# Kernel optimization log

Hardware: AMD Instinct MI355X
Metric: run time of the kernel (lower is better)

The kernel has to match this reference:

```python
import jax, jax.numpy as jnp
import numpy as np

B, N, DIM = 256, 196, 384
H, KD, VD = 12, 32, 32
RES = 14
EPS = 1e-5


def _build_bias_idxs():
    pts = [(i, j) for i in range(RES) for j in range(RES)]
    offs, idxs = {}, []
    for p1 in pts:
        for p2 in pts:
            o = (abs(p1[0] - p2[0]), abs(p1[1] - p2[1]))
            if o not in offs:
                offs[o] = len(offs)
            idxs.append(offs[o])
    return jnp.asarray(np.array(idxs, dtype=np.int32).reshape(N, N))


def setup_inputs() -> dict:
    key = jax.random.key(0)
    ks = jax.random.split(key, 4)
    return {
        "x": jax.random.normal(ks[0], (B, N, DIM), dtype=jnp.float32),
        "norm_w": jnp.ones((DIM,), jnp.float32),
        "norm_b": jnp.zeros((DIM,), jnp.float32),
        "qkv_w": jax.random.normal(ks[1], (H * (VD + 2 * KD), DIM), jnp.float32) * 0.02,
        "qkv_b": jnp.zeros((H * (VD + 2 * KD),), jnp.float32),
        "attention_biases": jax.random.normal(ks[2], (H, RES * RES), jnp.float32) * 0.02,
        "proj_w": jax.random.normal(ks[3], (DIM, H * VD), jnp.float32) * 0.02,
        "proj_b": jnp.zeros((DIM,), jnp.float32),
        "bias_idxs": _build_bias_idxs(),
    }


def reference(x, norm_w, norm_b, qkv_w, qkv_b, attention_biases, proj_w, proj_b, bias_idxs):
    scale = KD ** -0.5
    # LayerNorm over feature dim
    mu = jnp.mean(x, axis=-1, keepdims=True)
    var = jnp.mean(jnp.square(x - mu), axis=-1, keepdims=True)
    xn = (x - mu) * jax.lax.rsqrt(var + EPS) * norm_w + norm_b
    # QKV projection: [B,N,H*(2*KD+VD)] -> [B,N,H,*]
    qkv = (jnp.einsum("bnd,fd->bnf", xn, qkv_w) + qkv_b).reshape(B, N, H, 2 * KD + VD)
    q, k, v = qkv[..., :KD], qkv[..., KD:2 * KD], qkv[..., 2 * KD:]
    # Relative-position bias gathered into [H,N,N]
    attn_bias = attention_biases[:, bias_idxs]
    # Scores [B,H,N,N] with bias, softmax, AV
    scores = jnp.einsum("bnhk,bmhk->bhnm", q * scale, k) + attn_bias
    probs = jax.nn.softmax(scores, axis=-1)
    out = jnp.einsum("bhnm,bmhv->bnhv", probs, v).reshape(B, N, H * VD)
    return jnp.einsum("bnf,df->bnd", out, proj_w) + proj_b
```

## Files before the change

kernel.cpp:

```cpp
#include <hip/hip_runtime.h>

#define B_    256
#define N_    196
#define NP_   208
#define VSTR_ 264
#define DIM_  384
#define H_    12
#define KD_   32
#define VD_   32
#define F_    1152
#define ROWS_ (B_ * N_)
#define SCALE_ 0.17677669529663687f
#define EPS_  1e-5f

typedef __bf16 bf16_t;
typedef __bf16 bf16x2 __attribute__((ext_vector_type(2)));
typedef __bf16 bf16x4 __attribute__((ext_vector_type(4)));
typedef __bf16 bf16x8 __attribute__((ext_vector_type(8)));
typedef float  f32x4  __attribute__((ext_vector_type(4)));

__device__ __forceinline__ f32x4 mfma16(bf16x8 a, bf16x8 b, f32x4 c) {
    return __builtin_amdgcn_mfma_f32_16x16x32_bf16(a, b, c, 0, 0, 0);
}

__device__ __forceinline__ void gl2lds(const bf16_t* g, bf16_t* l) {
    __builtin_amdgcn_global_load_lds(
        (const __attribute__((address_space(1))) void*)g,
        (__attribute__((address_space(3))) void*)l, 16, 0, 0);
}

__global__ __launch_bounds__(256) void cvt_w(const float* __restrict__ src,
                                             bf16_t* __restrict__ dst) {
    const int i = (blockIdx.x * 256 + threadIdx.x) * 4;
    const float4 v = *(const float4*)(src + i);
    bf16x4 o = {(bf16_t)v.x, (bf16_t)v.y, (bf16_t)v.z, (bf16_t)v.w};
    *(bf16x4*)(dst + i) = o;
}

__global__ __launch_bounds__(256) void ln_kernel(const float* __restrict__ x,
                                                 const float* __restrict__ w,
                                                 const float* __restrict__ bvec,
                                                 bf16_t* __restrict__ xn) {
    const int lane = threadIdx.x & 63;
    const int row  = blockIdx.x * 4 + (threadIdx.x >> 6);
    const float* xr = x + (size_t)row * DIM_;
    const float4 a = *(const float4*)(xr + lane * 4);
    const float2 c = *(const float2*)(xr + 256 + lane * 2);
    float s  = a.x + a.y + a.z + a.w + c.x + c.y;
    float s2 = a.x*a.x + a.y*a.y + a.z*a.z + a.w*a.w + c.x*c.x + c.y*c.y;
    #pragma unroll
    for (int o = 32; o > 0; o >>= 1) {
        s  += __shfl_xor(s, o);
        s2 += __shfl_xor(s2, o);
    }
    const float mu = s * (1.f / 384.f);
    const float rs = rsqrtf(s2 * (1.f / 384.f) - mu * mu + EPS_);
    const float4 w4 = *(const float4*)(w + lane * 4);
    const float2 w2 = *(const float2*)(w + 256 + lane * 2);
    const float4 b4 = *(const float4*)(bvec + lane * 4);
    const float2 b2 = *(const float2*)(bvec + 256 + lane * 2);
    bf16_t* orow = xn + (size_t)row * DIM_;
    bf16x4 o4 = {(bf16_t)((a.x - mu) * rs * w4.x + b4.x),
                 (bf16_t)((a.y - mu) * rs * w4.y + b4.y),
                 (bf16_t)((a.z - mu) * rs * w4.z + b4.z),
                 (bf16_t)((a.w - mu) * rs * w4.w + b4.w)};
    *(bf16x4*)(orow + lane * 4) = o4;
    bf16x2 o2 = {(bf16_t)((c.x - mu) * rs * w2.x + b2.x),
                 (bf16_t)((c.y - mu) * rs * w2.y + b2.y)};
    *(bf16x2*)(orow + 256 + lane * 2) = o2;
}

__global__ __launch_bounds__(256) void bias_gather(const float* __restrict__ biases,
                                                   const int* __restrict__ idxs,
                                                   bf16_t* __restrict__ biasT) {
    const int e = blockIdx.x * 256 + threadIdx.x;
    if (e >= H_ * NP_ * NP_) return;
    const int h = e / (NP_ * NP_);
    const int r = e % (NP_ * NP_);
    const int m = r / NP_;
    const int q = r % NP_;
    const float v = (m < N_ && q < N_) ? biases[h * N_ + idxs[q * N_ + m]] : -1e30f;
    biasT[e] = (bf16_t)v;
}

template <typename OutT>
__global__ __launch_bounds__(256) void gemm_mfma(const bf16_t* __restrict__ A,
                                                 const bf16_t* __restrict__ Wt,
                                                 const float* __restrict__ bias,
                                                 OutT* __restrict__ C,
                                                 int M, int Nout, int K) {
    __shared__ __align__(16) bf16_t As[2][128][64];
    __shared__ __align__(16) bf16_t Bs[2][128][64];
    const int tid  = threadIdx.x;
    const int lane = tid & 63;
    const int wv   = tid >> 6;
    const int ln   = lane & 15;
    const int ko   = lane >> 4;
    const int wr   = (wv >> 1) * 64;
    const int wc   = (wv & 1) * 64;
    const size_t bm = (size_t)blockIdx.y * 128;
    const size_t bn = (size_t)blockIdx.x * 128;

    const int grow  = lane >> 3;
    const int gslot = (lane & 7) ^ grow;
    const int srow  = wv * 32 + grow;
    const bf16_t* gA = A  + (bm + srow) * K + gslot * 8;
    const bf16_t* gB = Wt + (bn + srow) * K + gslot * 8;
    const int ldst = wv * 4 * 512 + lane * 8;

    f32x4 acc[4][4];
    #pragma unroll
    for (int i = 0; i < 4; i++)
        #pragma unroll
        for (int j = 0; j < 4; j++)
            acc[i][j] = (f32x4){0.f, 0.f, 0.f, 0.f};

    bf16_t* As0 = &As[0][0][0];
    bf16_t* Bs0 = &Bs[0][0][0];

    #pragma unroll
    for (int j = 0; j < 4; j++) {
        gl2lds(gA + (size_t)j * 8 * K, As0 + ldst + j * 512);
        gl2lds(gB + (size_t)j * 8 * K, Bs0 + ldst + j * 512);
    }
    __syncthreads();

    const int ntiles = K >> 6;
    int cur = 0;
    for (int t = 0; t < ntiles; ++t) {
        if (t + 1 < ntiles) {
            const int k0 = (t + 1) << 6;
            bf16_t* dA = As0 + (cur ^ 1) * (128 * 64) + ldst;
            bf16_t* dB = Bs0 + (cur ^ 1) * (128 * 64) + ldst;
            #pragma unroll
            for (int j = 0; j < 4; j++) {
                gl2lds(gA + k0 + (size_t)j * 8 * K, dA + j * 512);
                gl2lds(gB + k0 + (size_t)j * 8 * K, dB + j * 512);
            }
        }
        #pragma unroll
        for (int kh = 0; kh < 2; kh++) {
            bf16x8 af[4], bfr[4];
            #pragma unroll
            for (int i = 0; i < 4; i++) {
                const int row = wr + i * 16 + ln;
                af[i] = *(const bf16x8*)&As[cur][row][(((kh << 2) | ko) ^ (ln & 7)) * 8];
            }
            #pragma unroll
            for (int j = 0; j < 4; j++) {
                const int row = wc + j * 16 + ln;
                bfr[j] = *(const bf16x8*)&Bs[cur][row][(((kh << 2) | ko) ^ (ln & 7)) * 8];
            }
            #pragma unroll
            for (int i = 0; i < 4; i++)
                #pragma unroll
                for (int j = 0; j < 4; j++)
                    acc[i][j] = mfma16(bfr[j], af[i], acc[i][j]);
        }
        __syncthreads();
        cur ^= 1;
    }

    #pragma unroll
    for (int j = 0; j < 4; j++) {
        const int jc = wc + j * 16 + ko * 4;
        const float4 b4 = *(const float4*)(bias + bn + jc);
        #pragma unroll
        for (int i = 0; i < 4; i++) {
            const size_t row = bm + wr + i * 16 + ln;
            const float v0 = acc[i][j][0] + b4.x;
            const float v1 = acc[i][j][1] + b4.y;
            const float v2 = acc[i][j][2] + b4.z;
            const float v3 = acc[i][j][3] + b4.w;
            OutT* dst = C + row * (size_t)Nout + bn + jc;
            if constexpr (sizeof(OutT) == 2) {
                bf16x4 o = {(bf16_t)v0, (bf16_t)v1, (bf16_t)v2, (bf16_t)v3};
                *(bf16x4*)dst = o;
            } else {
                float4 o = {v0, v1, v2, v3};
                *(float4*)dst = o;
            }
        }
    }
}

__global__ __launch_bounds__(256) void attn_mfma(const bf16_t* __restrict__ qkv,
                                                 const bf16_t* __restrict__ biasT,
                                                 bf16_t* __restrict__ out) {
    const int b = blockIdx.x / H_;
    const int h = blockIdx.x % H_;
    __shared__ __align__(16) bf16_t Ks[NP_][32];
    __shared__ __align__(16) bf16_t Vt[VD_][VSTR_];
    const int tid  = threadIdx.x;
    const int lane = tid & 63;
    const int wv   = tid >> 6;
    const int ln   = lane & 15;
    const int ko   = lane >> 4;

    {
        const int rsub = lane >> 2;
        const int col  = (lane & 3) * 8;
        for (int c = wv; c < 13; c += 4) {
            const int row  = c * 16 + rsub;
            const int srow = min(row, N_ - 1);
            gl2lds(qkv + ((size_t)(b * N_ + srow) * H_ + h) * 96 + KD_ + col,
                   &Ks[row][col]);
        }
    }
    if (tid < 224) {
        const int m  = tid;
        const int kk = (m & ~31) + ((m & 15) >> 2) * 8 + ((m >> 4) & 1) * 4 + (m & 3);
        const bf16_t* src = qkv + ((size_t)(b * N_ + min(m, N_ - 1)) * H_ + h) * 96 + 2 * KD_;
        #pragma unroll
        for (int c4 = 0; c4 < 4; c4++) {
            bf16x8 v8 = {bf16_t(0), bf16_t(0), bf16_t(0), bf16_t(0),
                         bf16_t(0), bf16_t(0), bf16_t(0), bf16_t(0)};
            if (m < N_) v8 = *(const bf16x8*)(src + c4 * 8);
            #pragma unroll
            for (int j = 0; j < 8; j++) Vt[c4 * 8 + j][kk] = v8[j];
        }
    }
    __syncthreads();

    bf16x8 kf[13];
    #pragma unroll
    for (int c = 0; c < 13; c++)
        kf[c] = *(const bf16x8*)&Ks[c * 16 + ln][ko * 8];

    for (int t = wv; t < 13; t += 4) {
        const int q    = t * 16 + ln;
        const int qrow = min(q, N_ - 1);
        const bf16x8 qf =
            *(const bf16x8*)(qkv + ((size_t)(b * N_ + qrow) * H_ + h) * 96 + ko * 8);

        f32x4 sc[13];
        __builtin_amdgcn_s_setprio(1);
        #pragma unroll
        for (int c = 0; c < 13; c++) {
            f32x4 z = {0.f, 0.f, 0.f, 0.f};
            sc[c] = mfma16(kf[c], qf, z);
        }
        __builtin_amdgcn_s_setprio(0);

        const bf16_t* bT = biasT + ((size_t)(h * NP_) + ko * 4) * NP_ + t * 16 + ln;
        float mx = -1e30f;
        #pragma unroll
        for (int c = 0; c < 13; c++)
            #pragma unroll
            for (int r = 0; r < 4; r++) {
                const float s = sc[c][r] * SCALE_ + (float)bT[(c * 16 + r) * NP_];
                sc[c][r] = s;
                mx = fmaxf(mx, s);
            }
        mx = fmaxf(mx, __shfl_xor(mx, 16));
        mx = fmaxf(mx, __shfl_xor(mx, 32));
        float sum = 0.f;
        #pragma unroll
        for (int c = 0; c < 13; c++)
            #pragma unroll
            for (int r = 0; r < 4; r++) {
                const float p = __expf(sc[c][r] - mx);
                sc[c][r] = p;
                sum += p;
            }
        sum += __shfl_xor(sum, 16);
        sum += __shfl_xor(sum, 32);
        const float inv = 1.f / sum;

        f32x4 o0 = {0.f, 0.f, 0.f, 0.f};
        f32x4 o1 = {0.f, 0.f, 0.f, 0.f};
        __builtin_amdgcn_s_setprio(1);
        #pragma unroll
        for (int g = 0; g < 7; g++) {
            bf16x8 pf;
            #pragma unroll
            for (int jj = 0; jj < 4; jj++) pf[jj] = (bf16_t)sc[2 * g][jj];
            if (g < 6) {
                #pragma unroll
                for (int jj = 0; jj < 4; jj++) pf[4 + jj] = (bf16_t)sc[2 * g + 1][jj];
            } else {
                pf[4] = bf16_t(0); pf[5] = bf16_t(0);
                pf[6] = bf16_t(0); pf[7] = bf16_t(0);
            }
            const bf16x8 v0 = *(const bf16x8*)&Vt[ln][g * 32 + ko * 8];
            const bf16x8 v1 = *(const bf16x8*)&Vt[16 + ln][g * 32 + ko * 8];
            o0 = mfma16(v0, pf, o0);
            o1 = mfma16(v1, pf, o1);
        }
        __builtin_amdgcn_s_setprio(0);

        if (q < N_) {
            bf16_t* dst = out + (size_t)(b * N_ + q) * DIM_ + h * VD_ + ko * 4;
            bf16x4 oa = {(bf16_t)(o0[0] * inv), (bf16_t)(o0[1] * inv),
                         (bf16_t)(o0[2] * inv), (bf16_t)(o0[3] * inv)};
            bf16x4 ob = {(bf16_t)(o1[0] * inv), (bf16_t)(o1[1] * inv),
                         (bf16_t)(o1[2] * inv), (bf16_t)(o1[3] * inv)};
            *(bf16x4*)dst = oa;
            *(bf16x4*)(dst + 16) = ob;
        }
    }
}

extern "C" void kernel_launch(void* const* d_in, const int* in_sizes, int n_in,
                              void* d_out, int out_size, void* d_ws, size_t ws_size,
                              hipStream_t stream) {
    const float* x        = (const float*)d_in[0];
    const float* norm_w   = (const float*)d_in[1];
    const float* norm_b   = (const float*)d_in[2];
    const float* qkv_w    = (const float*)d_in[3];
    const float* qkv_b    = (const float*)d_in[4];
    const float* att_bias = (const float*)d_in[5];
    const float* proj_w   = (const float*)d_in[6];
    const float* proj_b   = (const float*)d_in[7];
    const int*   bias_idx = (const int*)d_in[8];
    float* out = (float*)d_out;

    char* ws = (char*)d_ws;
    size_t off = 0;
    bf16_t* xn       = (bf16_t*)(ws + off); off += (size_t)ROWS_ * DIM_ * 2;
    bf16_t* qkvbuf   = (bf16_t*)(ws + off); off += (size_t)ROWS_ * F_ * 2;
    bf16_t* attn_out = (bf16_t*)(ws + off); off += (size_t)ROWS_ * DIM_ * 2;
    bf16_t* biasT    = (bf16_t*)(ws + off); off += (size_t)H_ * NP_ * NP_ * 2;
    bf16_t* wq_bf    = (bf16_t*)(ws + off); off += (size_t)F_ * DIM_ * 2;
    bf16_t* wp_bf    = (bf16_t*)(ws + off); off += (size_t)DIM_ * DIM_ * 2;

    cvt_w<<<(F_ * DIM_) / 1024, 256, 0, stream>>>(qkv_w, wq_bf);
    cvt_w<<<(DIM_ * DIM_) / 1024, 256, 0, stream>>>(proj_w, wp_bf);
    ln_kernel<<<ROWS_ / 4, 256, 0, stream>>>(x, norm_w, norm_b, xn);
    bias_gather<<<(H_ * NP_ * NP_ + 255) / 256, 256, 0, stream>>>(att_bias, bias_idx, biasT);
    gemm_mfma<bf16_t><<<dim3(F_ / 128, ROWS_ / 128), 256, 0, stream>>>(
        xn, wq_bf, qkv_b, qkvbuf, ROWS_, F_, DIM_);
    attn_mfma<<<B_ * H_, 256, 0, stream>>>(qkvbuf, biasT, attn_out);
    gemm_mfma<float><<<dim3(DIM_ / 128, ROWS_ / 128), 256, 0, stream>>>(
        attn_out, wp_bf, proj_b, out, ROWS_, DIM_, DIM_);
}
```

Before: 364.9 us.

## Fold bias into MFMA accumulator, drop softmax max, remap GEMM blocks per XCD

The relative-position bias is now stored as fp32, pre-divided by the softmax scale, and loaded straight into the MFMA accumulator. This removes the separate bias add. Softmax skips the max-subtraction pass and uses exp2 with a folded log2e scale, which removes the max reduction and its shuffles but risks overflow if scores were large. The GEMMs use a 1D grid remapped so that each XCD gets a contiguous M chunk, and they replace __syncthreads with explicit vmcnt waits plus barriers. The fp32 bias table doubles its memory traffic.

```diff
diff --git a/kernel.cpp b/kernel.cpp
--- a/kernel.cpp
+++ b/kernel.cpp
@@ -11,6 +11,8 @@
 #define F_    1152
 #define ROWS_ (B_ * N_)
 #define SCALE_ 0.17677669529663687f
+#define INVSCALE_ 5.656854249492381f
+#define SCALE2_ (SCALE_ * 1.4426950408889634f)
 #define EPS_  1e-5f
 
 typedef __bf16 bf16_t;
@@ -72,15 +74,16 @@
 
 __global__ __launch_bounds__(256) void bias_gather(const float* __restrict__ biases,
                                                    const int* __restrict__ idxs,
-                                                   bf16_t* __restrict__ biasT) {
+                                                   float* __restrict__ biasF) {
     const int e = blockIdx.x * 256 + threadIdx.x;
     if (e >= H_ * NP_ * NP_) return;
     const int h = e / (NP_ * NP_);
     const int r = e % (NP_ * NP_);
-    const int m = r / NP_;
-    const int q = r % NP_;
-    const float v = (m < N_ && q < N_) ? biases[h * N_ + idxs[q * N_ + m]] : -1e30f;
-    biasT[e] = (bf16_t)v;
+    const int q = r / NP_;
+    const int m = r % NP_;
+    const float v = (m < N_ && q < N_)
+        ? biases[h * N_ + idxs[q * N_ + m]] * INVSCALE_ : -3e30f;
+    biasF[e] = v;
 }
 
 template <typename OutT>
@@ -98,8 +101,15 @@
     const int ko   = lane >> 4;
     const int wr   = (wv >> 1) * 64;
     const int wc   = (wv & 1) * 64;
-    const size_t bm = (size_t)blockIdx.y * 128;
-    const size_t bn = (size_t)blockIdx.x * 128;
+
+    const int MBlk   = M >> 7;
+    const int mchunk = MBlk >> 3;
+    const int xcd    = blockIdx.x & 7;
+    const int pos    = blockIdx.x >> 3;
+    const int l_m    = xcd * mchunk + pos % mchunk;
+    const int l_n    = pos / mchunk;
+    const size_t bm  = (size_t)l_m * 128;
+    const size_t bn  = (size_t)l_n * 128;
 
     const int grow  = lane >> 3;
     const int gslot = (lane & 7) ^ grow;
@@ -123,7 +133,6 @@
         gl2lds(gA + (size_t)j * 8 * K, As0 + ldst + j * 512);
         gl2lds(gB + (size_t)j * 8 * K, Bs0 + ldst + j * 512);
     }
-    __syncthreads();
 
     const int ntiles = K >> 6;
     int cur = 0;
@@ -137,7 +146,11 @@
                 gl2lds(gA + k0 + (size_t)j * 8 * K, dA + j * 512);
                 gl2lds(gB + k0 + (size_t)j * 8 * K, dB + j * 512);
             }
-        }
+            asm volatile("s_waitcnt vmcnt(8)" ::: "memory");
+        } else {
+            asm volatile("s_waitcnt vmcnt(0)" ::: "memory");
+        }
+        __builtin_amdgcn_s_barrier();
         #pragma unroll
         for (int kh = 0; kh < 2; kh++) {
             bf16x8 af[4], bfr[4];
@@ -157,7 +170,7 @@
                 for (int j = 0; j < 4; j++)
                     acc[i][j] = mfma16(bfr[j], af[i], acc[i][j]);
         }
-        __syncthreads();
+        __builtin_amdgcn_s_barrier();
         cur ^= 1;
     }
 
@@ -185,7 +198,7 @@
 }
 
 __global__ __launch_bounds__(256) void attn_mfma(const bf16_t* __restrict__ qkv,
-                                                 const bf16_t* __restrict__ biasT,
+                                                 const float* __restrict__ biasF,
                                                  bf16_t* __restrict__ out) {
     const int b = blockIdx.x / H_;
     const int h = blockIdx.x % H_;
@@ -232,34 +245,23 @@
         const int qrow = min(q, N_ - 1);
         const bf16x8 qf =
             *(const bf16x8*)(qkv + ((size_t)(b * N_ + qrow) * H_ + h) * 96 + ko * 8);
+        const float* bq = biasF + ((size_t)h * NP_ + q) * NP_ + ko * 4;
 
         f32x4 sc[13];
         __builtin_amdgcn_s_setprio(1);
         #pragma unroll
         for (int c = 0; c < 13; c++) {
-            f32x4 z = {0.f, 0.f, 0.f, 0.f};
+            const f32x4 z = *(const f32x4*)(bq + c * 16);
             sc[c] = mfma16(kf[c], qf, z);
         }
         __builtin_amdgcn_s_setprio(0);
 
-        const bf16_t* bT = biasT + ((size_t)(h * NP_) + ko * 4) * NP_ + t * 16 + ln;
-        float mx = -1e30f;
+        float sum = 0.f;
         #pragma unroll
         for (int c = 0; c < 13; c++)
             #pragma unroll
             for (int r = 0; r < 4; r++) {
-                const float s = sc[c][r] * SCALE_ + (float)bT[(c * 16 + r) * NP_];
-                sc[c][r] = s;
-                mx = fmaxf(mx, s);
-            }
-        mx = fmaxf(mx, __shfl_xor(mx, 16));
-        mx = fmaxf(mx, __shfl_xor(mx, 32));
-        float sum = 0.f;
-        #pragma unroll
-        for (int c = 0; c < 13; c++)
-            #pragma unroll
-            for (int r = 0; r < 4; r++) {
-                const float p = __expf(sc[c][r] - mx);
+                const float p = exp2f(sc[c][r] * SCALE2_);
                 sc[c][r] = p;
                 sum += p;
             }
@@ -320,17 +322,17 @@
     bf16_t* xn       = (bf16_t*)(ws + off); off += (size_t)ROWS_ * DIM_ * 2;
     bf16_t* qkvbuf   = (bf16_t*)(ws + off); off += (size_t)ROWS_ * F_ * 2;
     bf16_t* attn_out = (bf16_t*)(ws + off); off += (size_t)ROWS_ * DIM_ * 2;
-    bf16_t* biasT    = (bf16_t*)(ws + off); off += (size_t)H_ * NP_ * NP_ * 2;
+    float*  biasF    = (float*)(ws + off);  off += (size_t)H_ * NP_ * NP_ * 4;
     bf16_t* wq_bf    = (bf16_t*)(ws + off); off += (size_t)F_ * DIM_ * 2;
     bf16_t* wp_bf    = (bf16_t*)(ws + off); off += (size_t)DIM_ * DIM_ * 2;
 
     cvt_w<<<(F_ * DIM_) / 1024, 256, 0, stream>>>(qkv_w, wq_bf);
     cvt_w<<<(DIM_ * DIM_) / 1024, 256, 0, stream>>>(proj_w, wp_bf);
     ln_kernel<<<ROWS_ / 4, 256, 0, stream>>>(x, norm_w, norm_b, xn);
-    bias_gather<<<(H_ * NP_ * NP_ + 255) / 256, 256, 0, stream>>>(att_bias, bias_idx, biasT);
-    gemm_mfma<bf16_t><<<dim3(F_ / 128, ROWS_ / 128), 256, 0, stream>>>(
+    bias_gather<<<(H_ * NP_ * NP_ + 255) / 256, 256, 0, stream>>>(att_bias, bias_idx, biasF);
+    gemm_mfma<bf16_t><<<(ROWS_ / 128) * (F_ / 128), 256, 0, stream>>>(
         xn, wq_bf, qkv_b, qkvbuf, ROWS_, F_, DIM_);
-    attn_mfma<<<B_ * H_, 256, 0, stream>>>(qkvbuf, biasT, attn_out);
-    gemm_mfma<float><<<dim3(DIM_ / 128, ROWS_ / 128), 256, 0, stream>>>(
+    attn_mfma<<<B_ * H_, 256, 0, stream>>>(qkvbuf, biasF, attn_out);
+    gemm_mfma<float><<<(ROWS_ / 128) * (DIM_ / 128), 256, 0, stream>>>(
         attn_out, wp_bf, proj_b, out, ROWS_, DIM_, DIM_);
 }
```

After: 380.4 us. 1.04x slower.
